# Optimization experiments

Hardware: AMD Instinct MI355X
Metric: run time of the kernel (lower is better)

The kernel has to match this reference:

```python
import jax, jax.numpy as jnp
import numpy as np

N_NODES = 10000
N_EDGES = 160000
N_FEATS = 9       # OGB atom features
VOCAB = 128       # >= max atom feature cardinality (119)
D = 128           # d_input == d_atom_emb
H = 4             # n_heads
C = 128           # out_channels per head (== d_input)
L = 3             # n_layers
N_CLASSES = 10
NEG_SLOPE = 0.2   # PyG GATConv default


def setup_inputs() -> dict:
    key = jax.random.key(0)
    ks = jax.random.split(key, 10)
    nodes_features = jax.random.randint(ks[0], (N_NODES, N_FEATS), 0, 119, dtype=jnp.int64)
    edges_connectivity = jax.random.randint(ks[1], (2, N_EDGES), 0, N_NODES, dtype=jnp.int64)
    s = 1.0 / np.sqrt(D)
    emb_tables = jax.random.normal(ks[2], (N_FEATS, VOCAB, D), dtype=jnp.float32) * s
    W = jax.random.normal(ks[3], (L, D, H * C), dtype=jnp.float32) * s
    att_src = jax.random.normal(ks[4], (L, H, C), dtype=jnp.float32) * s
    att_dst = jax.random.normal(ks[5], (L, H, C), dtype=jnp.float32) * s
    bias = jnp.zeros((L, C), dtype=jnp.float32)
    Wc = jax.random.normal(ks[6], (D, N_CLASSES), dtype=jnp.float32) * s
    bc = jnp.zeros((N_CLASSES,), dtype=jnp.float32)
    return {"nodes_features": nodes_features, "edges_connectivity": edges_connectivity,
            "emb_tables": emb_tables, "W": W, "att_src": att_src, "att_dst": att_dst,
            "bias": bias, "Wc": Wc, "bc": bc}


def _gat_layer(x, src, dst, W_l, a_s, a_d, b_l):
    # x: [N, D] -> h: [N, H, C]
    h = (x @ W_l).reshape(-1, H, C)
    alpha_src = jnp.einsum('nhc,hc->nh', h, a_s)  # [N, H]
    alpha_dst = jnp.einsum('nhc,hc->nh', h, a_d)  # [N, H]
    e = alpha_src[src] + alpha_dst[dst]           # [E, H]
    e = jnp.where(e >= 0, e, NEG_SLOPE * e)       # LeakyReLU(0.2)
    # segment softmax over edges grouped by destination node
    m = jax.ops.segment_max(e, dst, num_segments=N_NODES)  # [N, H]
    ex = jnp.exp(e - m[dst])
    s = jax.ops.segment_sum(ex, dst, num_segments=N_NODES)  # [N, H]
    alpha = ex / (s[dst] + 1e-16)                 # [E, H]
    msg = h[src] * alpha[..., None]               # [E, H, C]
    out = jax.ops.segment_sum(msg, dst, num_segments=N_NODES)  # [N, H, C]
    return out.mean(axis=1) + b_l                 # concat=False: mean over heads


def reference(nodes_features, edges_connectivity, emb_tables, W, att_src, att_dst, bias, Wc, bc):
    # AtomEncoder: sum per-feature embeddings -> [N, D]
    x = emb_tables[jnp.arange(N_FEATS), nodes_features].sum(axis=1)
    src, dst = edges_connectivity[0], edges_connectivity[1]
    for i in range(L):
        # dropout treated as identity (eval-mode reference)
        x = _gat_layer(x, src, dst, W[i], att_src[i], att_dst[i], bias[i])
        if i < L - 1:
            x = jax.nn.gelu(x)
    pooled = x.mean(axis=0)                       # graph mean-pool over nodes -> [D]
    return pooled @ Wc + bc                       # [n_classes]
```

## Files before the change

### kernel.cpp

```cpp
#include <hip/hip_runtime.h>
#include <hip/hip_bf16.h>
#include <math.h>

#define NN 10000
#define NE 160000
#define NF 9
#define VOCAB 128
#define D 128
#define NH 4
#define C 128
#define HC 512
#define NCLS 10
#define NL 3

#define NEG_BIG (-1e30f)

typedef __attribute__((ext_vector_type(8))) short bf16x8;
typedef __attribute__((ext_vector_type(4))) float f32x4;

__device__ __forceinline__ unsigned short f2bf(float f) {
    unsigned u = __float_as_uint(f);
    unsigned r = ((u >> 16) & 1u) + 0x7FFFu;
    return (unsigned short)((u + r) >> 16);
}
__device__ __forceinline__ float bf2f(unsigned short h) {
    return __uint_as_float(((unsigned)h) << 16);
}

__global__ __launch_bounds__(256)
void hist(const int* __restrict__ dst, int* __restrict__ deg) {
    int e = blockIdx.x * 256 + threadIdx.x;
    if (e < NE) atomicAdd(&deg[dst[e]], 1);
}

#define SCAN_T 1024
#define SCAN_PER ((NN + SCAN_T - 1) / SCAN_T)
__global__ __launch_bounds__(SCAN_T)
void scan_deg(const int* __restrict__ deg, int* __restrict__ rowstart,
              int* __restrict__ cursor) {
    __shared__ int part[SCAN_T];
    int t = threadIdx.x;
    int base = t * SCAN_PER;
    int vals[SCAN_PER];
    int loc = 0;
#pragma unroll
    for (int i = 0; i < SCAN_PER; ++i) {
        int idx = base + i;
        int v = (idx < NN) ? deg[idx] : 0;
        vals[i] = v;
        loc += v;
    }
    part[t] = loc;
    __syncthreads();
    for (int off = 1; off < SCAN_T; off <<= 1) {
        int y = (t >= off) ? part[t - off] : 0;
        __syncthreads();
        part[t] += y;
        __syncthreads();
    }
    int run = part[t] - loc;
#pragma unroll
    for (int i = 0; i < SCAN_PER; ++i) {
        int idx = base + i;
        if (idx < NN) { rowstart[idx] = run; cursor[idx] = run; }
        run += vals[i];
    }
}

__global__ __launch_bounds__(256)
void scatter(const int* __restrict__ src, const int* __restrict__ dst,
             int* __restrict__ cursor, int* __restrict__ csr_src) {
    int e = blockIdx.x * 256 + threadIdx.x;
    if (e < NE) {
        int p = atomicAdd(&cursor[dst[e]], 1);
        csr_src[p] = src[e];
    }
}

__global__ __launch_bounds__(512)
void prep_all(const float* __restrict__ W, const float* __restrict__ as_,
              const float* __restrict__ ad_, const float* __restrict__ Wc,
              const float* __restrict__ biasA, const float* __restrict__ bc,
              float* __restrict__ wsrc, float* __restrict__ wdst,
              unsigned short* __restrict__ Bth, unsigned short* __restrict__ Btl,
              float* __restrict__ M, float* __restrict__ b10,
              float* __restrict__ p512) {
    int b = blockIdx.x;
    if (b < 24) {
        int k = threadIdx.x;
        if (k >= 128) return;
        int l = b >> 3;
        int r = b & 7;
        int h = r >> 1;
        int side = r & 1;
        const float* av = (side ? ad_ : as_) + (size_t)(l * NH + h) * C;
        const float* wrow = W + (size_t)l * D * HC + (size_t)k * HC + h * C;
        float acc = 0.f;
#pragma unroll 4
        for (int c = 0; c < C; ++c) acc += wrow[c] * av[c];
        float* o = (side ? wdst : wsrc) + (size_t)(l * NH + h) * D + k;
        *o = acc;
    } else if (b < 280) {
        int bb = b - 24;
        int l = bb >> 7;
        int c = bb & 127;
        int j = threadIdx.x;
        float v = W[(size_t)l * D * HC + (size_t)(j >> 2) * HC + (j & 3) * C + c];
        unsigned short h = f2bf(v);
        unsigned short lo = f2bf(v - bf2f(h));
        size_t o = (size_t)(l * 128 + c) * HC + j;
        Bth[o] = h;
        Btl[o] = lo;
    } else {
        int k = b - 280;
        int j = threadIdx.x;
        const float* W3 = W + (size_t)2 * D * HC;
        const float* bias3 = biasA + (size_t)2 * D;
        const float* wrow = W3 + (size_t)(j >> 2) * HC + (j & 3) * C;
        float acc = 0.f;
#pragma unroll 4
        for (int c = 0; c < C; ++c) acc += wrow[c] * Wc[c * NCLS + k];
        M[(size_t)k * HC + j] = acc;
        if (k == 0) p512[j] = 0.f;
        if (j == 0) {
            float bsum = bc[k];
            for (int c = 0; c < C; ++c) bsum += bias3[c] * Wc[c * NCLS + k];
            b10[k] = bsum;
        }
    }
}

__global__ __launch_bounds__(128)
void atom_encoder_alpha(const int* __restrict__ feats, const float* __restrict__ emb,
                        const float* __restrict__ wsrc0, const float* __restrict__ wdst0,
                        float* __restrict__ x, float* __restrict__ asrc,
                        float* __restrict__ adst) {
    int n = blockIdx.x;
    int t = threadIdx.x;
    __shared__ int f[NF];
    __shared__ float part[2][8];
    if (t < NF) f[t] = feats[n * NF + t];
    __syncthreads();
    float acc = 0.f;
#pragma unroll
    for (int i = 0; i < NF; ++i)
        acc += emb[(i * VOCAB + f[i]) * D + t];
    x[n * D + t] = acc;

    float dots[8];
#pragma unroll
    for (int h = 0; h < NH; ++h) {
        dots[h]     = acc * wsrc0[h * D + t];
        dots[4 + h] = acc * wdst0[h * D + t];
    }
#pragma unroll
    for (int off = 32; off; off >>= 1)
#pragma unroll
        for (int k = 0; k < 8; ++k) dots[k] += __shfl_down(dots[k], off);
    if ((t & 63) == 0) {
        int w = t >> 6;
#pragma unroll
        for (int k = 0; k < 8; ++k) part[w][k] = dots[k];
    }
    __syncthreads();
    if (t < 8) {
        float v = part[0][t] + part[1][t];
        if (t < 4) asrc[n * NH + t] = v;
        else       adst[n * NH + (t - 4)] = v;
    }
}

__global__ __launch_bounds__(256)
void alphas2(const float* __restrict__ X, const float* __restrict__ wsrc,
             const float* __restrict__ wdst, float* __restrict__ asrc,
             float* __restrict__ adst) {
    int n = blockIdx.x * 4 + (threadIdx.x >> 6);
    int lane = threadIdx.x & 63;
    float x0 = X[n * D + lane], x1 = X[n * D + lane + 64];
#pragma unroll
    for (int h = 0; h < NH; ++h) {
        float s = x0 * wsrc[h * D + lane] + x1 * wsrc[h * D + lane + 64];
        float d = x0 * wdst[h * D + lane] + x1 * wdst[h * D + lane + 64];
#pragma unroll
        for (int off = 32; off; off >>= 1) {
            s += __shfl_down(s, off);
            d += __shfl_down(d, off);
        }
        if (lane == 0) { asrc[n * NH + h] = s; adst[n * NH + h] = d; }
    }
}

__global__ __launch_bounds__(128)
void gat_agg(const int* __restrict__ csr_src, const int* __restrict__ rowstart,
             const int* __restrict__ degA, const float* __restrict__ asr,
             const float* __restrict__ adr, const float* __restrict__ X,
             unsigned* __restrict__ aggh, unsigned* __restrict__ aggl) {
    int n = blockIdx.x;
    int t = threadIdx.x;
    int deg = degA[n];
    int start = rowstart[n];

    __shared__ float smax[NH];
    __shared__ float sinv[NH];
    __shared__ float lal[128][NH];
    __shared__ int lsrc[128];

    int h = t >> 5, i = t & 31;
    float ad_h = adr[n * NH + h];
    float mx = NEG_BIG;
    for (int j = i; j < deg; j += 32) {
        int s = csr_src[start + j];
        float v = asr[s * NH + h] + ad_h;
        v = v >= 0.f ? v : 0.2f * v;
        mx = fmaxf(mx, v);
    }
#pragma unroll
    for (int off = 16; off; off >>= 1) mx = fmaxf(mx, __shfl_xor(mx, off));
    if (i == 0) smax[h] = mx;
    __syncthreads();
    float m = smax[h];
    float ss = 0.f;
    for (int j = i; j < deg; j += 32) {
        int s = csr_src[start + j];
        float v = asr[s * NH + h] + ad_h;
        v = v >= 0.f ? v : 0.2f * v;
        ss += __expf(v - m);
    }
#pragma unroll
    for (int off = 16; off; off >>= 1) ss += __shfl_xor(ss, off);
    if (i == 0) sinv[h] = 0.25f / (ss + 1e-16f);
    __syncthreads();

    float fm0 = smax[0], fm1 = smax[1], fm2 = smax[2], fm3 = smax[3];
    float fi0 = sinv[0], fi1 = sinv[1], fi2 = sinv[2], fi3 = sinv[3];
    float a0 = adr[n * NH + 0], a1 = adr[n * NH + 1];
    float a2 = adr[n * NH + 2], a3 = adr[n * NH + 3];
    float acc0 = 0.f, acc1 = 0.f, acc2 = 0.f, acc3 = 0.f;

    for (int cb = 0; cb < deg; cb += 128) {
        int cl = deg - cb; if (cl > 128) cl = 128;
        if (t < cl) {
            int sn = csr_src[start + cb + t];
            float4 av = *(const float4*)(asr + sn * NH);
            float v0 = av.x + a0; v0 = v0 >= 0.f ? v0 : 0.2f * v0;
            float v1 = av.y + a1; v1 = v1 >= 0.f ? v1 : 0.2f * v1;
            float v2 = av.z + a2; v2 = v2 >= 0.f ? v2 : 0.2f * v2;
            float v3 = av.w + a3; v3 = v3 >= 0.f ? v3 : 0.2f * v3;
            lal[t][0] = __expf(v0 - fm0) * fi0;
            lal[t][1] = __expf(v1 - fm1) * fi1;
            lal[t][2] = __expf(v2 - fm2) * fi2;
            lal[t][3] = __expf(v3 - fm3) * fi3;
            lsrc[t] = sn;
        }
        __syncthreads();
#pragma unroll 4
        for (int j = 0; j < cl; ++j) {
            float xv = X[(size_t)lsrc[j] * D + t];
            float4 w = *(const float4*)lal[j];
            acc0 += w.x * xv;
            acc1 += w.y * xv;
            acc2 += w.z * xv;
            acc3 += w.w * xv;
        }
        __syncthreads();
    }

    unsigned short h0 = f2bf(acc0), h1 = f2bf(acc1), h2 = f2bf(acc2), h3 = f2bf(acc3);
    unsigned short l0 = f2bf(acc0 - bf2f(h0)), l1 = f2bf(acc1 - bf2f(h1));
    unsigned short l2 = f2bf(acc2 - bf2f(h2)), l3 = f2bf(acc3 - bf2f(h3));
    size_t base = ((size_t)n * HC + t * 4) >> 1;
    uint2 uh = make_uint2((unsigned)h0 | ((unsigned)h1 << 16),
                          (unsigned)h2 | ((unsigned)h3 << 16));
    uint2 ul = make_uint2((unsigned)l0 | ((unsigned)l1 << 16),
                          (unsigned)l2 | ((unsigned)l3 << 16));
    *(uint2*)(aggh + base) = uh;
    *(uint2*)(aggl + base) = ul;
}

__global__ __launch_bounds__(64)
void gemm_mfma(const unsigned short* __restrict__ Ah, const unsigned short* __restrict__ Al,
               const unsigned short* __restrict__ Bth, const unsigned short* __restrict__ Btl,
               const float* __restrict__ bias, float* __restrict__ Out, int do_gelu) {
    int lane = threadIdx.x;
    int m0 = blockIdx.x * 16;
    int n0 = blockIdx.y * 64;
    int r = lane & 15;
    int g = lane >> 4;

    const bf16x8* ah = (const bf16x8*)(Ah + (size_t)(m0 + r) * HC + g * 8);
    const bf16x8* al = (const bf16x8*)(Al + (size_t)(m0 + r) * HC + g * 8);
    const bf16x8* bh0 = (const bf16x8*)(Bth + (size_t)(n0 + 0 * 16 + r) * HC + g * 8);
    const bf16x8* bh1 = (const bf16x8*)(Bth + (size_t)(n0 + 1 * 16 + r) * HC + g * 8);
    const bf16x8* bh2 = (const bf16x8*)(Bth + (size_t)(n0 + 2 * 16 + r) * HC + g * 8);
    const bf16x8* bh3 = (const bf16x8*)(Bth + (size_t)(n0 + 3 * 16 + r) * HC + g * 8);
    const bf16x8* bl0 = (const bf16x8*)(Btl + (size_t)(n0 + 0 * 16 + r) * HC + g * 8);
    const bf16x8* bl1 = (const bf16x8*)(Btl + (size_t)(n0 + 1 * 16 + r) * HC + g * 8);
    const bf16x8* bl2 = (const bf16x8*)(Btl + (size_t)(n0 + 2 * 16 + r) * HC + g * 8);
    const bf16x8* bl3 = (const bf16x8*)(Btl + (size_t)(n0 + 3 * 16 + r) * HC + g * 8);

    f32x4 acc[4];
#pragma unroll
    for (int q = 0; q < 4; ++q) acc[q] = (f32x4){0.f, 0.f, 0.f, 0.f};

#pragma unroll 2
    for (int ks = 0; ks < HC / 32; ++ks) {
        bf16x8 a_h = ah[ks * 4];
        bf16x8 a_l = al[ks * 4];
        bf16x8 b;
        b = bh0[ks * 4];
        acc[0] = __builtin_amdgcn_mfma_f32_16x16x32_bf16(a_h, b, acc[0], 0, 0, 0);
        acc[0] = __builtin_amdgcn_mfma_f32_16x16x32_bf16(a_l, b, acc[0], 0, 0, 0);
        b = bl0[ks * 4];
        acc[0] = __builtin_amdgcn_mfma_f32_16x16x32_bf16(a_h, b, acc[0], 0, 0, 0);
        b = bh1[ks * 4];
        acc[1] = __builtin_amdgcn_mfma_f32_16x16x32_bf16(a_h, b, acc[1], 0, 0, 0);
        acc[1] = __builtin_amdgcn_mfma_f32_16x16x32_bf16(a_l, b, acc[1], 0, 0, 0);
        b = bl1[ks * 4];
        acc[1] = __builtin_amdgcn_mfma_f32_16x16x32_bf16(a_h, b, acc[1], 0, 0, 0);
        b = bh2[ks * 4];
        acc[2] = __builtin_amdgcn_mfma_f32_16x16x32_bf16(a_h, b, acc[2], 0, 0, 0);
        acc[2] = __builtin_amdgcn_mfma_f32_16x16x32_bf16(a_l, b, acc[2], 0, 0, 0);
        b = bl2[ks * 4];
        acc[2] = __builtin_amdgcn_mfma_f32_16x16x32_bf16(a_h, b, acc[2], 0, 0, 0);
        b = bh3[ks * 4];
        acc[3] = __builtin_amdgcn_mfma_f32_16x16x32_bf16(a_h, b, acc[3], 0, 0, 0);
        acc[3] = __builtin_amdgcn_mfma_f32_16x16x32_bf16(a_l, b, acc[3], 0, 0, 0);
        b = bl3[ks * 4];
        acc[3] = __builtin_amdgcn_mfma_f32_16x16x32_bf16(a_h, b, acc[3], 0, 0, 0);
    }

#pragma unroll
    for (int q = 0; q < 4; ++q) {
#pragma unroll
        for (int i = 0; i < 4; ++i) {
            int row = m0 + g * 4 + i;
            int col = n0 + q * 16 + r;
            float v = acc[q][i] + bias[col];
            if (do_gelu) {
                float u = 0.7978845608028654f * (v + 0.044715f * v * v * v);
                v = 0.5f * v * (1.f + tanhf(u));
            }
            Out[(size_t)row * D + col] = v;
        }
    }
}

__global__ __launch_bounds__(512)
void pool512(const unsigned short* __restrict__ Ah, const unsigned short* __restrict__ Al,
             float* __restrict__ p) {
    int t = threadIdx.x;
    int chunk = (NN + gridDim.x - 1) / gridDim.x;
    int n0 = blockIdx.x * chunk;
    int n1 = n0 + chunk; if (n1 > NN) n1 = NN;
    float acc = 0.f;
    for (int n = n0; n < n1; ++n)
        acc += bf2f(Ah[(size_t)n * HC + t]) + bf2f(Al[(size_t)n * HC + t]);
    atomicAdd(p + t, acc);
}

__global__ __launch_bounds__(640)
void final10(const float* __restrict__ p512, const float* __restrict__ M,
             const float* __restrict__ b10, float* __restrict__ out) {
    int k = threadIdx.x >> 6;
    int lane = threadIdx.x & 63;
    float acc = 0.f;
#pragma unroll
    for (int i = 0; i < HC / 64; ++i) {
        int j = lane + i * 64;
        acc += p512[j] * M[(size_t)k * HC + j];
    }
#pragma unroll
    for (int off = 32; off; off >>= 1) acc += __shfl_down(acc, off);
    if (lane == 0) out[k] = b10[k] + acc * (1.0f / NN);
}

extern "C" void kernel_launch(void* const* d_in, const int* in_sizes, int n_in,
                              void* d_out, int out_size, void* d_ws, size_t ws_size,
                              hipStream_t stream) {
    const int*   feats = (const int*)d_in[0];
    const int*   edges = (const int*)d_in[1];
    const float* emb   = (const float*)d_in[2];
    const float* W     = (const float*)d_in[3];
    const float* asrcW = (const float*)d_in[4];
    const float* adstW = (const float*)d_in[5];
    const float* bias  = (const float*)d_in[6];
    const float* Wc    = (const float*)d_in[7];
    const float* bc    = (const float*)d_in[8];
    float* out = (float*)d_out;

    const int* srcp = edges;
    const int* dstp = edges + NE;

    char* ws = (char*)d_ws;
    size_t off = 0;
    unsigned short* aggh = (unsigned short*)(ws + off); off += (size_t)NN * HC * 2;
    unsigned short* aggl = (unsigned short*)(ws + off); off += (size_t)NN * HC * 2;
    float* xb0    = (float*)(ws + off); off += (size_t)NN * D * 4;
    float* xb1    = (float*)(ws + off); off += (size_t)NN * D * 4;
    float* asrc   = (float*)(ws + off); off += (size_t)NN * NH * 4;
    float* adst   = (float*)(ws + off); off += (size_t)NN * NH * 4;
    int*   deg    = (int*)(ws + off);   off += (size_t)NN * 4;
    int*   rowst  = (int*)(ws + off);   off += (size_t)NN * 4;
    int*   cursor = (int*)(ws + off);   off += (size_t)NN * 4;
    int*   csrsrc = (int*)(ws + off);   off += (size_t)NE * 4;
    float* wsrcb  = (float*)(ws + off); off += (size_t)NL * NH * D * 4;
    float* wdstb  = (float*)(ws + off); off += (size_t)NL * NH * D * 4;
    unsigned short* Bth = (unsigned short*)(ws + off); off += (size_t)2 * 128 * HC * 2;
    unsigned short* Btl = (unsigned short*)(ws + off); off += (size_t)2 * 128 * HC * 2;
    float* Mhead  = (float*)(ws + off); off += (size_t)NCLS * HC * 4;
    float* b10    = (float*)(ws + off); off += NCLS * 4;
    float* p512   = (float*)(ws + off); off += HC * 4;

    hipMemsetAsync(deg, 0, (size_t)NN * 4, stream);
    hist<<<(NE + 255) / 256, 256, 0, stream>>>(dstp, deg);
    scan_deg<<<1, SCAN_T, 0, stream>>>(deg, rowst, cursor);
    scatter<<<(NE + 255) / 256, 256, 0, stream>>>(srcp, dstp, cursor, csrsrc);
    prep_all<<<290, 512, 0, stream>>>(W, asrcW, adstW, Wc, bias, bc,
                                      wsrcb, wdstb, Bth, Btl, Mhead, b10, p512);

    atom_encoder_alpha<<<NN, 128, 0, stream>>>(feats, emb, wsrcb, wdstb,
                                               xb0, asrc, adst);

    float* xin = xb0;
    float* xout = xb1;
    for (int l = 0; l < 2; ++l) {
        if (l > 0)
            alphas2<<<NN / 4, 256, 0, stream>>>(xin, wsrcb + (size_t)l * NH * D,
                                                wdstb + (size_t)l * NH * D, asrc, adst);
        gat_agg<<<NN, 128, 0, stream>>>(csrsrc, rowst, deg, asrc, adst, xin,
                                        (unsigned*)aggh, (unsigned*)aggl);
        gemm_mfma<<<dim3(NN / 16, 2), 64, 0, stream>>>(
            aggh, aggl, Bth + (size_t)l * 128 * HC, Btl + (size_t)l * 128 * HC,
            bias + (size_t)l * D, xout, 1);
        float* tmp = xin; xin = xout; xout = tmp;
    }

    alphas2<<<NN / 4, 256, 0, stream>>>(xin, wsrcb + (size_t)2 * NH * D,
                                        wdstb + (size_t)2 * NH * D, asrc, adst);
    gat_agg<<<NN, 128, 0, stream>>>(csrsrc, rowst, deg, asrc, adst, xin,
                                    (unsigned*)aggh, (unsigned*)aggl);
    pool512<<<100, 512, 0, stream>>>(aggh, aggl, p512);
    final10<<<1, 640, 0, stream>>>(p512, Mhead, b10, out);
}
```

Before: 296.7 us.

## Fuse attention-logit computation into GEMM epilogue and merge pool with final head

The GEMM kernel now runs both 64-column halves in one 128-thread block, stages the GELU output tile in shared memory, and computes the next layer's per-node source and destination attention logits in the epilogue. This removes the separate alphas2 launches and the re-read of X. The pooling kernel uses a last-block-done atomic counter to compute the final 10-class projection itself, which drops the final10 launch. The cost is extra shared memory and a serial 128-element dot product per thread in the GEMM, plus a counter that must be reset on every call.

```diff
diff --git a/kernel.cpp b/kernel.cpp
--- a/kernel.cpp
+++ b/kernel.cpp
@@ -84,7 +84,7 @@
               float* __restrict__ wsrc, float* __restrict__ wdst,
               unsigned short* __restrict__ Bth, unsigned short* __restrict__ Btl,
               float* __restrict__ M, float* __restrict__ b10,
-              float* __restrict__ p512) {
+              float* __restrict__ p512, int* __restrict__ done) {
     int b = blockIdx.x;
     if (b < 24) {
         int k = threadIdx.x;
@@ -122,6 +122,7 @@
         for (int c = 0; c < C; ++c) acc += wrow[c] * Wc[c * NCLS + k];
         M[(size_t)k * HC + j] = acc;
         if (k == 0) p512[j] = 0.f;
+        if (k == 0 && j == 0) *done = 0;
         if (j == 0) {
             float bsum = bc[k];
             for (int c = 0; c < C; ++c) bsum += bias3[c] * Wc[c * NCLS + k];
@@ -167,26 +168,6 @@
         float v = part[0][t] + part[1][t];
         if (t < 4) asrc[n * NH + t] = v;
         else       adst[n * NH + (t - 4)] = v;
-    }
-}
-
-__global__ __launch_bounds__(256)
-void alphas2(const float* __restrict__ X, const float* __restrict__ wsrc,
-             const float* __restrict__ wdst, float* __restrict__ asrc,
-             float* __restrict__ adst) {
-    int n = blockIdx.x * 4 + (threadIdx.x >> 6);
-    int lane = threadIdx.x & 63;
-    float x0 = X[n * D + lane], x1 = X[n * D + lane + 64];
-#pragma unroll
-    for (int h = 0; h < NH; ++h) {
-        float s = x0 * wsrc[h * D + lane] + x1 * wsrc[h * D + lane + 64];
-        float d = x0 * wdst[h * D + lane] + x1 * wdst[h * D + lane + 64];
-#pragma unroll
-        for (int off = 32; off; off >>= 1) {
-            s += __shfl_down(s, off);
-            d += __shfl_down(d, off);
-        }
-        if (lane == 0) { asrc[n * NH + h] = s; adst[n * NH + h] = d; }
     }
 }
 
@@ -277,13 +258,19 @@
     *(uint2*)(aggl + base) = ul;
 }
 
-__global__ __launch_bounds__(64)
-void gemm_mfma(const unsigned short* __restrict__ Ah, const unsigned short* __restrict__ Al,
-               const unsigned short* __restrict__ Bth, const unsigned short* __restrict__ Btl,
-               const float* __restrict__ bias, float* __restrict__ Out, int do_gelu) {
-    int lane = threadIdx.x;
+__global__ __launch_bounds__(128)
+void gemm_mfma_alpha(const unsigned short* __restrict__ Ah, const unsigned short* __restrict__ Al,
+                     const unsigned short* __restrict__ Bth, const unsigned short* __restrict__ Btl,
+                     const float* __restrict__ bias,
+                     const float* __restrict__ wsrcN, const float* __restrict__ wdstN,
+                     float* __restrict__ Out, float* __restrict__ asrc,
+                     float* __restrict__ adst) {
+    __shared__ float s_out[16][132];
+    int tid = threadIdx.x;
+    int lane = tid & 63;
+    int wvid = tid >> 6;
     int m0 = blockIdx.x * 16;
-    int n0 = blockIdx.y * 64;
+    int n0 = wvid * 64;
     int r = lane & 15;
     int g = lane >> 4;
 
@@ -333,21 +320,31 @@
     for (int q = 0; q < 4; ++q) {
 #pragma unroll
         for (int i = 0; i < 4; ++i) {
-            int row = m0 + g * 4 + i;
+            int row = g * 4 + i;
             int col = n0 + q * 16 + r;
             float v = acc[q][i] + bias[col];
-            if (do_gelu) {
-                float u = 0.7978845608028654f * (v + 0.044715f * v * v * v);
-                v = 0.5f * v * (1.f + tanhf(u));
-            }
-            Out[(size_t)row * D + col] = v;
+            float u = 0.7978845608028654f * (v + 0.044715f * v * v * v);
+            v = 0.5f * v * (1.f + tanhf(u));
+            Out[(size_t)(m0 + row) * D + col] = v;
+            s_out[row][col] = v;
         }
     }
+    __syncthreads();
+
+    int row = tid >> 3;
+    int k = tid & 7;
+    const float* wvp = (k < 4) ? (wsrcN + k * D) : (wdstN + (k - 4) * D);
+    float dacc = 0.f;
+#pragma unroll 8
+    for (int c = 0; c < 128; ++c) dacc += s_out[row][c] * wvp[c];
+    if (k < 4) asrc[(m0 + row) * NH + k] = dacc;
+    else       adst[(m0 + row) * NH + (k - 4)] = dacc;
 }
 
 __global__ __launch_bounds__(512)
-void pool512(const unsigned short* __restrict__ Ah, const unsigned short* __restrict__ Al,
-             float* __restrict__ p) {
+void pool_final(const unsigned short* __restrict__ Ah, const unsigned short* __restrict__ Al,
+                const float* __restrict__ M, const float* __restrict__ b10,
+                float* __restrict__ p, int* __restrict__ done, float* __restrict__ out) {
     int t = threadIdx.x;
     int chunk = (NN + gridDim.x - 1) / gridDim.x;
     int n0 = blockIdx.x * chunk;
@@ -356,22 +353,29 @@
     for (int n = n0; n < n1; ++n)
         acc += bf2f(Ah[(size_t)n * HC + t]) + bf2f(Al[(size_t)n * HC + t]);
     atomicAdd(p + t, acc);
-}
-
-__global__ __launch_bounds__(640)
-void final10(const float* __restrict__ p512, const float* __restrict__ M,
-             const float* __restrict__ b10, float* __restrict__ out) {
-    int k = threadIdx.x >> 6;
-    int lane = threadIdx.x & 63;
-    float acc = 0.f;
-#pragma unroll
-    for (int i = 0; i < HC / 64; ++i) {
-        int j = lane + i * 64;
-        acc += p512[j] * M[(size_t)k * HC + j];
-    }
-#pragma unroll
-    for (int off = 32; off; off >>= 1) acc += __shfl_down(acc, off);
-    if (lane == 0) out[k] = b10[k] + acc * (1.0f / NN);
+    __threadfence();
+
+    __shared__ int isLast;
+    if (t == 0) {
+        int old = atomicAdd(done, 1);
+        isLast = (old == (int)gridDim.x - 1) ? 1 : 0;
+    }
+    __syncthreads();
+    if (isLast) {
+        __threadfence();
+        int k = t >> 4, i = t & 15;
+        if (k < NCLS) {
+            float a2 = 0.f;
+#pragma unroll 8
+            for (int q = 0; q < HC / 16; ++q) {
+                int j = i + q * 16;
+                a2 += p[j] * M[(size_t)k * HC + j];
+            }
+#pragma unroll
+            for (int off = 8; off; off >>= 1) a2 += __shfl_down(a2, off, 16);
+            if (i == 0) out[k] = b10[k] + a2 * (1.0f / NN);
+        }
+    }
 }
 
 extern "C" void kernel_launch(void* const* d_in, const int* in_sizes, int n_in,
@@ -410,35 +414,33 @@
     float* Mhead  = (float*)(ws + off); off += (size_t)NCLS * HC * 4;
     float* b10    = (float*)(ws + off); off += NCLS * 4;
     float* p512   = (float*)(ws + off); off += HC * 4;
+    int*   done   = (int*)(ws + off);   off += 4;
 
     hipMemsetAsync(deg, 0, (size_t)NN * 4, stream);
     hist<<<(NE + 255) / 256, 256, 0, stream>>>(dstp, deg);
     scan_deg<<<1, SCAN_T, 0, stream>>>(deg, rowst, cursor);
     scatter<<<(NE + 255) / 256, 256, 0, stream>>>(srcp, dstp, cursor, csrsrc);
     prep_all<<<290, 512, 0, stream>>>(W, asrcW, adstW, Wc, bias, bc,
-                                      wsrcb, wdstb, Bth, Btl, Mhead, b10, p512);
+                                      wsrcb, wdstb, Bth, Btl, Mhead, b10, p512, done);
 
     atom_encoder_alpha<<<NN, 128, 0, stream>>>(feats, emb, wsrcb, wdstb,
                                                xb0, asrc, adst);
 
-    float* xin = xb0;
-    float* xout = xb1;
-    for (int l = 0; l < 2; ++l) {
-        if (l > 0)
-            alphas2<<<NN / 4, 256, 0, stream>>>(xin, wsrcb + (size_t)l * NH * D,
-                                                wdstb + (size_t)l * NH * D, asrc, adst);
-        gat_agg<<<NN, 128, 0, stream>>>(csrsrc, rowst, deg, asrc, adst, xin,
-                                        (unsigned*)aggh, (unsigned*)aggl);
-        gemm_mfma<<<dim3(NN / 16, 2), 64, 0, stream>>>(
-            aggh, aggl, Bth + (size_t)l * 128 * HC, Btl + (size_t)l * 128 * HC,
-            bias + (size_t)l * D, xout, 1);
-        float* tmp = xin; xin = xout; xout = tmp;
-    }
-
-    alphas2<<<NN / 4, 256, 0, stream>>>(xin, wsrcb + (size_t)2 * NH * D,
-                                        wdstb + (size_t)2 * NH * D, asrc, adst);
-    gat_agg<<<NN, 128, 0, stream>>>(csrsrc, rowst, deg, asrc, adst, xin,
+    gat_agg<<<NN, 128, 0, stream>>>(csrsrc, rowst, deg, asrc, adst, xb0,
                                     (unsigned*)aggh, (unsigned*)aggl);
-    pool512<<<100, 512, 0, stream>>>(aggh, aggl, p512);
-    final10<<<1, 640, 0, stream>>>(p512, Mhead, b10, out);
-}
+    gemm_mfma_alpha<<<NN / 16, 128, 0, stream>>>(
+        aggh, aggl, Bth, Btl, bias,
+        wsrcb + (size_t)1 * NH * D, wdstb + (size_t)1 * NH * D,
+        xb1, asrc, adst);
+
+    gat_agg<<<NN, 128, 0, stream>>>(csrsrc, rowst, deg, asrc, adst, xb1,
+                                    (unsigned*)aggh, (unsigned*)aggl);
+    gemm_mfma_alpha<<<NN / 16, 128, 0, stream>>>(
+        aggh, aggl, Bth + (size_t)128 * HC, Btl + (size_t)128 * HC, bias + (size_t)1 * D,
+        wsrcb + (size_t)2 * NH * D, wdstb + (size_t)2 * NH * D,
+        xb0, asrc, adst);
+
+    gat_agg<<<NN, 128, 0, stream>>>(csrsrc, rowst, deg, asrc, adst, xb0,
+                                    (unsigned*)aggh, (unsigned*)aggl);
+    pool_final<<<100, 512, 0, stream>>>(aggh, aggl, Mhead, b10, p512, done, out);
+}
```

After: 314.0 us. 1.06x slower.
